# Kernel tuning notes

Hardware: AMD Instinct MI355X
Metric: run time of the kernel (lower is better)

## Reference

```python
import jax, jax.numpy as jnp
import numpy as np
import math

N = 8192
IN_FEATURES = 512
OUT_FEATURES = 64
NEG_INF = -9e15

def setup_inputs() -> dict:
    key = jax.random.key(0)
    k1, k2, k3, k4 = jax.random.split(key, 4)
    inp = jax.random.normal(k1, (N, IN_FEATURES), dtype=jnp.float32)
    adj = jax.random.randint(k2, (N, N), 0, 2, dtype=jnp.int32)
    # xavier_uniform with gain=1.414 for [in, out] weights
    limit = 1.414 * math.sqrt(6.0 / (IN_FEATURES + OUT_FEATURES))
    kW = jax.random.uniform(k3, (IN_FEATURES, OUT_FEATURES), dtype=jnp.float32, minval=-limit, maxval=limit)
    vW = jax.random.uniform(k4, (IN_FEATURES, OUT_FEATURES), dtype=jnp.float32, minval=-limit, maxval=limit)
    return {"input": inp, "adj": adj, "kW": kW, "vW": vW}

def reference(input, adj, kW, vW):
    kh = input @ kW                      # [N, d]
    vh = input @ vW                      # [N, d]
    d = kh.shape[1]
    K = (kh @ kh.T) / jnp.sqrt(jnp.asarray(d, dtype=kh.dtype))  # [N, N]
    scores = jnp.where(adj > 0, K, jnp.asarray(NEG_INF, dtype=K.dtype))
    attention = jax.nn.softmax(scores, axis=1)
    # dropout is a no-op (p=0.0 / eval mode)
    h_prime = attention @ vh             # [N, d]
    return jax.nn.elu(h_prime)           # concat=True path
```

## Files before the change

kernel.cpp:

```cpp
#include <hip/hip_runtime.h>
#include <math.h>

typedef __bf16 bf16_t;
typedef __bf16 bf16x8 __attribute__((ext_vector_type(8)));
typedef float f32x4 __attribute__((ext_vector_type(4)));

#define NN 8192
#define L2E 1.44269504088896340736f
#define SMAX 45.0f
#define KSCALE 0.35355339059327373f
#define ACCW 66

__global__ __launch_bounds__(256) void proj_kernel(
    const float* __restrict__ input,
    const float* __restrict__ kW,
    const float* __restrict__ vW,
    bf16_t* __restrict__ khs_hi,
    bf16_t* __restrict__ khs_lo,
    bf16_t* __restrict__ vhT)
{
    __shared__ __align__(16) bf16_t WkH[64][136];
    __shared__ __align__(16) bf16_t WkL[64][136];
    __shared__ __align__(16) bf16_t WvH[64][136];
    __shared__ __align__(16) bf16_t WvL[64][136];

    const int tid   = threadIdx.x;
    const int wv    = tid >> 6;
    const int lane  = tid & 63;
    const int l15   = lane & 15;
    const int quad  = lane >> 4;
    const int rbase = blockIdx.x * 64 + wv * 16;

    f32x4 kacc[4] = {};
    f32x4 vacc[4] = {};

    for (int kk = 0; kk < 4; ++kk) {
        __syncthreads();
        #pragma unroll
        for (int i = 0; i < 32; ++i) {
            int idx = tid + i * 256;
            int kl  = idx >> 6;
            int n   = idx & 63;
            float wk  = kW[(kk * 128 + kl) * 64 + n];
            float wv2 = vW[(kk * 128 + kl) * 64 + n];
            bf16_t kh = (bf16_t)wk;
            bf16_t vh = (bf16_t)wv2;
            WkH[n][kl] = kh;  WkL[n][kl] = (bf16_t)(wk - (float)kh);
            WvH[n][kl] = vh;  WvL[n][kl] = (bf16_t)(wv2 - (float)vh);
        }
        __syncthreads();

        #pragma unroll
        for (int kc = 0; kc < 4; ++kc) {
            const float* ap = &input[(size_t)(rbase + l15) * 512 + kk * 128 + kc * 32 + quad * 8];
            f32x4 a0 = *(const f32x4*)ap;
            f32x4 a1 = *(const f32x4*)(ap + 4);
            bf16x8 ah, al;
            #pragma unroll
            for (int j = 0; j < 4; ++j) {
                bf16_t h0 = (bf16_t)a0[j], h1 = (bf16_t)a1[j];
                ah[j]     = h0;  al[j]     = (bf16_t)(a0[j] - (float)h0);
                ah[4 + j] = h1;  al[4 + j] = (bf16_t)(a1[j] - (float)h1);
            }
            #pragma unroll
            for (int nb = 0; nb < 4; ++nb) {
                bf16x8 bkh = *(const bf16x8*)&WkH[nb * 16 + l15][kc * 32 + quad * 8];
                bf16x8 bkl = *(const bf16x8*)&WkL[nb * 16 + l15][kc * 32 + quad * 8];
                bf16x8 bvh = *(const bf16x8*)&WvH[nb * 16 + l15][kc * 32 + quad * 8];
                bf16x8 bvl = *(const bf16x8*)&WvL[nb * 16 + l15][kc * 32 + quad * 8];
                kacc[nb] = __builtin_amdgcn_mfma_f32_16x16x32_bf16(ah, bkh, kacc[nb], 0, 0, 0);
                kacc[nb] = __builtin_amdgcn_mfma_f32_16x16x32_bf16(al, bkh, kacc[nb], 0, 0, 0);
                kacc[nb] = __builtin_amdgcn_mfma_f32_16x16x32_bf16(ah, bkl, kacc[nb], 0, 0, 0);
                vacc[nb] = __builtin_amdgcn_mfma_f32_16x16x32_bf16(ah, bvh, vacc[nb], 0, 0, 0);
                vacc[nb] = __builtin_amdgcn_mfma_f32_16x16x32_bf16(al, bvh, vacc[nb], 0, 0, 0);
                vacc[nb] = __builtin_amdgcn_mfma_f32_16x16x32_bf16(ah, bvl, vacc[nb], 0, 0, 0);
            }
        }
    }

    #pragma unroll
    for (int nb = 0; nb < 4; ++nb) {
        const int dcol = nb * 16 + l15;
        #pragma unroll
        for (int r = 0; r < 4; ++r) {
            float v  = kacc[nb][r] * KSCALE;
            bf16_t h = (bf16_t)v;
            khs_hi[(size_t)(rbase + quad * 4 + r) * 64 + dcol] = h;
            khs_lo[(size_t)(rbase + quad * 4 + r) * 64 + dcol] = (bf16_t)(v - (float)h);
        }
        union { bf16_t b[4]; uint2 u; } pk;
        #pragma unroll
        for (int r = 0; r < 4; ++r) pk.b[r] = (bf16_t)vacc[nb][r];
        *(uint2*)&vhT[(size_t)dcol * NN + rbase + quad * 4] = pk.u;
    }
}

__global__ void zero_acc(float* __restrict__ acc) {
    int i = blockIdx.x * blockDim.x + threadIdx.x;
    if (i < NN * ACCW) acc[i] = 0.f;
}

__global__ __launch_bounds__(512, 4) void attn_kernel(
    const int* __restrict__ adj,
    const bf16_t* __restrict__ khs_hi,
    const bf16_t* __restrict__ khs_lo,
    const bf16_t* __restrict__ vhT,
    float* __restrict__ acc)
{
    __shared__ __align__(16) float PlBuf[8 * 1152];

    const int tid   = threadIdx.x;
    const int w     = tid >> 6;
    const int lane  = tid & 63;
    const int l15   = lane & 15;
    const int quad  = lane >> 4;
    const int rb    = blockIdx.x >> 1;
    const int ch    = blockIdx.x & 1;
    const int qbase = rb * 16;
    const int colstart = ch * 4096 + w * 512;

    const bf16x8 qh0 = *(const bf16x8*)&khs_hi[(size_t)(qbase + l15) * 64 + quad * 8];
    const bf16x8 qh1 = *(const bf16x8*)&khs_hi[(size_t)(qbase + l15) * 64 + 32 + quad * 8];
    const bf16x8 ql0 = *(const bf16x8*)&khs_lo[(size_t)(qbase + l15) * 64 + quad * 8];
    const bf16x8 ql1 = *(const bf16x8*)&khs_lo[(size_t)(qbase + l15) * 64 + 32 + quad * 8];

    bf16x8 ones;
    #pragma unroll
    for (int j = 0; j < 8; ++j) ones[j] = (bf16_t)1.0f;

    f32x4 o0 = {}, o1 = {}, o2 = {}, o3 = {}, o4 = {};

    const int* aptr = adj + (size_t)(qbase + quad * 4) * NN + colstart + l15;

    int acur[8], anxt[8];
    #pragma unroll
    for (int r = 0; r < 4; ++r) {
        acur[2 * r]     = aptr[(size_t)r * NN];
        acur[2 * r + 1] = aptr[(size_t)r * NN + 16];
    }

    for (int t = 0; t < 16; ++t) {
        const int colbase = colstart + t * 32;
        float* Plw = &PlBuf[w * 1152 + (t & 1) * 576];

        const bf16_t* kph = khs_hi + (size_t)(colbase + l15) * 64 + quad * 8;
        bf16x8 bh00 = *(const bf16x8*)(kph);
        bf16x8 bh01 = *(const bf16x8*)(kph + 32);
        bf16x8 bh10 = *(const bf16x8*)(kph + 16 * 64);
        bf16x8 bh11 = *(const bf16x8*)(kph + 16 * 64 + 32);
        const bf16_t* vp = vhT + (size_t)l15 * NN + colbase + quad * 8;
        bf16x8 bv0 = *(const bf16x8*)(vp);
        bf16x8 bv1 = *(const bf16x8*)(vp + (size_t)16 * NN);
        bf16x8 bv2 = *(const bf16x8*)(vp + (size_t)32 * NN);
        bf16x8 bv3 = *(const bf16x8*)(vp + (size_t)48 * NN);

        const int cnx = ((t + 1) & 15) * 32;
        #pragma unroll
        for (int r = 0; r < 4; ++r) {
            anxt[2 * r]     = aptr[(size_t)r * NN + cnx];
            anxt[2 * r + 1] = aptr[(size_t)r * NN + cnx + 16];
        }

        f32x4 zz = {};
        f32x4 s0 = __builtin_amdgcn_mfma_f32_16x16x32_bf16(qh0, bh00, zz, 0, 0, 0);
        s0 = __builtin_amdgcn_mfma_f32_16x16x32_bf16(qh1, bh01, s0, 0, 0, 0);
        s0 = __builtin_amdgcn_mfma_f32_16x16x32_bf16(ql0, bh00, s0, 0, 0, 0);
        s0 = __builtin_amdgcn_mfma_f32_16x16x32_bf16(ql1, bh01, s0, 0, 0, 0);
        f32x4 s1 = __builtin_amdgcn_mfma_f32_16x16x32_bf16(qh0, bh10, zz, 0, 0, 0);
        s1 = __builtin_amdgcn_mfma_f32_16x16x32_bf16(qh1, bh11, s1, 0, 0, 0);
        s1 = __builtin_amdgcn_mfma_f32_16x16x32_bf16(ql0, bh10, s1, 0, 0, 0);
        s1 = __builtin_amdgcn_mfma_f32_16x16x32_bf16(ql1, bh11, s1, 0, 0, 0);

        #pragma unroll
        for (int r = 0; r < 4; ++r) {
            float p0 = acur[2 * r]     > 0 ? __builtin_amdgcn_exp2f((s0[r] - SMAX) * L2E) : 0.f;
            float p1 = acur[2 * r + 1] > 0 ? __builtin_amdgcn_exp2f((s1[r] - SMAX) * L2E) : 0.f;
            Plw[(quad * 4 + r) * 36 + l15]      = p0;
            Plw[(quad * 4 + r) * 36 + 16 + l15] = p1;
        }

        __asm__ __volatile__("s_waitcnt lgkmcnt(0)" ::: "memory");

        f32x4 pfa = *(const f32x4*)&Plw[l15 * 36 + quad * 8];
        f32x4 pfb = *(const f32x4*)&Plw[l15 * 36 + quad * 8 + 4];
        bf16x8 pa;
        #pragma unroll
        for (int j = 0; j < 4; ++j) { pa[j] = (bf16_t)pfa[j]; pa[4 + j] = (bf16_t)pfb[j]; }

        o0 = __builtin_amdgcn_mfma_f32_16x16x32_bf16(pa, bv0, o0, 0, 0, 0);
        o1 = __builtin_amdgcn_mfma_f32_16x16x32_bf16(pa, bv1, o1, 0, 0, 0);
        o2 = __builtin_amdgcn_mfma_f32_16x16x32_bf16(pa, bv2, o2, 0, 0, 0);
        o3 = __builtin_amdgcn_mfma_f32_16x16x32_bf16(pa, bv3, o3, 0, 0, 0);
        o4 = __builtin_amdgcn_mfma_f32_16x16x32_bf16(pa, ones, o4, 0, 0, 0);

        #pragma unroll
        for (int i = 0; i < 8; ++i) acur[i] = anxt[i];
    }

    float* M = PlBuf;
    #pragma unroll
    for (int s = 4; s >= 1; s >>= 1) {
        __syncthreads();
        if (w >= s && w < 2 * s) {
            float* base = M + (w - s) * 16 * 68;
            #pragma unroll
            for (int r = 0; r < 4; ++r) {
                const int row = quad * 4 + r;
                base[row * 68 + l15]      = o0[r];
                base[row * 68 + 16 + l15] = o1[r];
                base[row * 68 + 32 + l15] = o2[r];
                base[row * 68 + 48 + l15] = o3[r];
                if (l15 == 0) base[row * 68 + 64] = o4[r];
            }
        }
        __syncthreads();
        if (w < s) {
            float* base = M + w * 16 * 68;
            #pragma unroll
            for (int r = 0; r < 4; ++r) {
                const int row = quad * 4 + r;
                o0[r] += base[row * 68 + l15];
                o1[r] += base[row * 68 + 16 + l15];
                o2[r] += base[row * 68 + 32 + l15];
                o3[r] += base[row * 68 + 48 + l15];
                o4[r] += base[row * 68 + 64];
            }
        }
    }

    if (w == 0) {
        #pragma unroll
        for (int r = 0; r < 4; ++r) {
            const size_t row = (size_t)qbase + quad * 4 + r;
            atomicAdd(&acc[row * ACCW + l15],      o0[r]);
            atomicAdd(&acc[row * ACCW + 16 + l15], o1[r]);
            atomicAdd(&acc[row * ACCW + 32 + l15], o2[r]);
            atomicAdd(&acc[row * ACCW + 48 + l15], o3[r]);
            if (l15 == 0) atomicAdd(&acc[row * ACCW + 64], o4[r]);
        }
    }
}

__global__ void finalize(const float* __restrict__ acc, float* __restrict__ out) {
    int i = blockIdx.x * blockDim.x + threadIdx.x;
    int row = i >> 6, d = i & 63;
    float l = acc[(size_t)row * ACCW + 64];
    float v = acc[(size_t)row * ACCW + d] / (l > 0.f ? l : 1.f);
    out[i] = v > 0.f ? v : expm1f(v);
}

extern "C" void kernel_launch(void* const* d_in, const int* in_sizes, int n_in,
                              void* d_out, int out_size, void* d_ws, size_t ws_size,
                              hipStream_t stream) {
    const float* input = nullptr;
    const int*   adj   = nullptr;
    const float* kW    = nullptr;
    const float* vW    = nullptr;
    for (int i = 0; i < n_in; ++i) {
        if (in_sizes[i] == 8192 * 512)            input = (const float*)d_in[i];
        else if (in_sizes[i] == 512 * 64) {
            if (!kW) kW = (const float*)d_in[i]; else vW = (const float*)d_in[i];
        } else                                    adj = (const int*)d_in[i];
    }
    float* out = (float*)d_out;

    bf16_t* khs_hi = (bf16_t*)d_ws;
    bf16_t* khs_lo = khs_hi + (size_t)NN * 64;
    bf16_t* vhT    = khs_lo + (size_t)NN * 64;
    float*  acc    = (float*)((char*)d_ws + 3u * 1024 * 1024);

    zero_acc<<<(NN * ACCW + 255) / 256, 256, 0, stream>>>(acc);
    proj_kernel<<<128, 256, 0, stream>>>(input, kW, vW, khs_hi, khs_lo, vhT);
    attn_kernel<<<1024, 512, 0, stream>>>(adj, khs_hi, khs_lo, vhT, acc);
    finalize<<<(NN * 64) / 512, 512, 0, stream>>>(acc, out);
}
```

Before: 517.7 us.

## Pack adjacency into bitmask, drop split-K atomics and fuse finalize into attention

Adds a pre-pass kernel that ballots the int32 adjacency matrix into a 1-bit-per-entry mask. The attention kernel then reads 32 mask bits per word instead of 32 int32 values. The attention grid no longer splits columns across two blocks: each block's 8 waves cover all 8192 columns. That removes the zero-init kernel, the global float atomics and the separate finalize kernel, and the normalization and ELU now run in the epilogue. The projection kernel moves to 128-thread blocks over 32 rows. The trade-off is an extra full pass over the adjacency matrix, plus half as many attention blocks, each with twice the serial work, which may lower occupancy.

```diff
diff --git a/kernel.cpp b/kernel.cpp
--- a/kernel.cpp
+++ b/kernel.cpp
@@ -9,9 +9,27 @@
 #define L2E 1.44269504088896340736f
 #define SMAX 45.0f
 #define KSCALE 0.35355339059327373f
-#define ACCW 66
-
-__global__ __launch_bounds__(256) void proj_kernel(
+
+__global__ __launch_bounds__(256) void pack_adj(
+    const int* __restrict__ adj, unsigned int* __restrict__ bits)
+{
+    const int lane = threadIdx.x & 63;
+    const int gw   = blockIdx.x * 4 + (threadIdx.x >> 6);
+    const int nw   = gridDim.x * 4;
+    const int nchunks = (NN / 256) * NN;
+    for (int c = gw; c < nchunks; c += nw) {
+        const int* p = adj + (size_t)c * 256;
+        unsigned int* o = bits + (size_t)c * 8;
+        #pragma unroll
+        for (int k = 0; k < 4; ++k) {
+            int v = p[k * 64 + lane];
+            unsigned long long m = __ballot(v > 0);
+            if (lane == 0) *(uint2*)(o + 2 * k) = *(uint2*)&m;
+        }
+    }
+}
+
+__global__ __launch_bounds__(128) void proj_kernel(
     const float* __restrict__ input,
     const float* __restrict__ kW,
     const float* __restrict__ vW,
@@ -29,16 +47,16 @@
     const int lane  = tid & 63;
     const int l15   = lane & 15;
     const int quad  = lane >> 4;
-    const int rbase = blockIdx.x * 64 + wv * 16;
+    const int rbase = blockIdx.x * 32 + wv * 16;
 
     f32x4 kacc[4] = {};
     f32x4 vacc[4] = {};
 
     for (int kk = 0; kk < 4; ++kk) {
         __syncthreads();
-        #pragma unroll
-        for (int i = 0; i < 32; ++i) {
-            int idx = tid + i * 256;
+        #pragma unroll 16
+        for (int i = 0; i < 64; ++i) {
+            int idx = tid + i * 128;
             int kl  = idx >> 6;
             int n   = idx & 63;
             float wk  = kW[(kk * 128 + kl) * 64 + n];
@@ -95,17 +113,12 @@
     }
 }
 
-__global__ void zero_acc(float* __restrict__ acc) {
-    int i = blockIdx.x * blockDim.x + threadIdx.x;
-    if (i < NN * ACCW) acc[i] = 0.f;
-}
-
 __global__ __launch_bounds__(512, 4) void attn_kernel(
-    const int* __restrict__ adj,
+    const unsigned int* __restrict__ bits,
     const bf16_t* __restrict__ khs_hi,
     const bf16_t* __restrict__ khs_lo,
     const bf16_t* __restrict__ vhT,
-    float* __restrict__ acc)
+    float* __restrict__ out)
 {
     __shared__ __align__(16) float PlBuf[8 * 1152];
 
@@ -114,10 +127,8 @@
     const int lane  = tid & 63;
     const int l15   = lane & 15;
     const int quad  = lane >> 4;
-    const int rb    = blockIdx.x >> 1;
-    const int ch    = blockIdx.x & 1;
-    const int qbase = rb * 16;
-    const int colstart = ch * 4096 + w * 512;
+    const int qbase = blockIdx.x * 16;
+    const int colstart = w * 1024;
 
     const bf16x8 qh0 = *(const bf16x8*)&khs_hi[(size_t)(qbase + l15) * 64 + quad * 8];
     const bf16x8 qh1 = *(const bf16x8*)&khs_hi[(size_t)(qbase + l15) * 64 + 32 + quad * 8];
@@ -130,16 +141,13 @@
 
     f32x4 o0 = {}, o1 = {}, o2 = {}, o3 = {}, o4 = {};
 
-    const int* aptr = adj + (size_t)(qbase + quad * 4) * NN + colstart + l15;
-
-    int acur[8], anxt[8];
-    #pragma unroll
-    for (int r = 0; r < 4; ++r) {
-        acur[2 * r]     = aptr[(size_t)r * NN];
-        acur[2 * r + 1] = aptr[(size_t)r * NN + 16];
-    }
-
-    for (int t = 0; t < 16; ++t) {
+    const unsigned int* bp = bits + (size_t)(qbase + quad * 4) * 256 + (colstart >> 5);
+
+    unsigned int wcur[4], wnxt[4];
+    #pragma unroll
+    for (int r = 0; r < 4; ++r) wcur[r] = bp[r * 256];
+
+    for (int t = 0; t < 32; ++t) {
         const int colbase = colstart + t * 32;
         float* Plw = &PlBuf[w * 1152 + (t & 1) * 576];
 
@@ -154,12 +162,9 @@
         bf16x8 bv2 = *(const bf16x8*)(vp + (size_t)32 * NN);
         bf16x8 bv3 = *(const bf16x8*)(vp + (size_t)48 * NN);
 
-        const int cnx = ((t + 1) & 15) * 32;
-        #pragma unroll
-        for (int r = 0; r < 4; ++r) {
-            anxt[2 * r]     = aptr[(size_t)r * NN + cnx];
-            anxt[2 * r + 1] = aptr[(size_t)r * NN + cnx + 16];
-        }
+        const int tn = (t + 1) & 31;
+        #pragma unroll
+        for (int r = 0; r < 4; ++r) wnxt[r] = bp[r * 256 + tn];
 
         f32x4 zz = {};
         f32x4 s0 = __builtin_amdgcn_mfma_f32_16x16x32_bf16(qh0, bh00, zz, 0, 0, 0);
@@ -173,8 +178,8 @@
 
         #pragma unroll
         for (int r = 0; r < 4; ++r) {
-            float p0 = acur[2 * r]     > 0 ? __builtin_amdgcn_exp2f((s0[r] - SMAX) * L2E) : 0.f;
-            float p1 = acur[2 * r + 1] > 0 ? __builtin_amdgcn_exp2f((s1[r] - SMAX) * L2E) : 0.f;
+            float p0 = ((wcur[r] >> l15) & 1u)        ? __builtin_amdgcn_exp2f((s0[r] - SMAX) * L2E) : 0.f;
+            float p1 = ((wcur[r] >> (16 + l15)) & 1u) ? __builtin_amdgcn_exp2f((s1[r] - SMAX) * L2E) : 0.f;
             Plw[(quad * 4 + r) * 36 + l15]      = p0;
             Plw[(quad * 4 + r) * 36 + 16 + l15] = p1;
         }
@@ -194,7 +199,7 @@
         o4 = __builtin_amdgcn_mfma_f32_16x16x32_bf16(pa, ones, o4, 0, 0, 0);
 
         #pragma unroll
-        for (int i = 0; i < 8; ++i) acur[i] = anxt[i];
+        for (int r = 0; r < 4; ++r) wcur[r] = wnxt[r];
     }
 
     float* M = PlBuf;
@@ -232,21 +237,15 @@
         #pragma unroll
         for (int r = 0; r < 4; ++r) {
             const size_t row = (size_t)qbase + quad * 4 + r;
-            atomicAdd(&acc[row * ACCW + l15],      o0[r]);
-            atomicAdd(&acc[row * ACCW + 16 + l15], o1[r]);
-            atomicAdd(&acc[row * ACCW + 32 + l15], o2[r]);
-            atomicAdd(&acc[row * ACCW + 48 + l15], o3[r]);
-            if (l15 == 0) atomicAdd(&acc[row * ACCW + 64], o4[r]);
-        }
-    }
-}
-
-__global__ void finalize(const float* __restrict__ acc, float* __restrict__ out) {
-    int i = blockIdx.x * blockDim.x + threadIdx.x;
-    int row = i >> 6, d = i & 63;
-    float l = acc[(size_t)row * ACCW + 64];
-    float v = acc[(size_t)row * ACCW + d] / (l > 0.f ? l : 1.f);
-    out[i] = v > 0.f ? v : expm1f(v);
+            float l   = o4[r];
+            float inv = 1.0f / (l > 0.f ? l : 1.0f);
+            float v0 = o0[r] * inv, v1 = o1[r] * inv, v2 = o2[r] * inv, v3 = o3[r] * inv;
+            out[row * 64 + l15]      = v0 > 0.f ? v0 : expm1f(v0);
+            out[row * 64 + 16 + l15] = v1 > 0.f ? v1 : expm1f(v1);
+            out[row * 64 + 32 + l15] = v2 > 0.f ? v2 : expm1f(v2);
+            out[row * 64 + 48 + l15] = v3 > 0.f ? v3 : expm1f(v3);
+        }
+    }
 }
 
 extern "C" void kernel_launch(void* const* d_in, const int* in_sizes, int n_in,
@@ -267,10 +266,9 @@
     bf16_t* khs_hi = (bf16_t*)d_ws;
     bf16_t* khs_lo = khs_hi + (size_t)NN * 64;
     bf16_t* vhT    = khs_lo + (size_t)NN * 64;
-    float*  acc    = (float*)((char*)d_ws + 3u * 1024 * 1024);
-
-    zero_acc<<<(NN * ACCW + 255) / 256, 256, 0, stream>>>(acc);
-    proj_kernel<<<128, 256, 0, stream>>>(input, kW, vW, khs_hi, khs_lo, vhT);
-    attn_kernel<<<1024, 512, 0, stream>>>(adj, khs_hi, khs_lo, vhT, acc);
-    finalize<<<(NN * 64) / 512, 512, 0, stream>>>(acc, out);
-}
+    unsigned int* bits = (unsigned int*)((char*)d_ws + 3u * 1024 * 1024);
+
+    pack_adj<<<2048, 256, 0, stream>>>(adj, bits);
+    proj_kernel<<<256, 128, 0, stream>>>(input, kW, vW, khs_hi, khs_lo, vhT);
+    attn_kernel<<<512, 512, 0, stream>>>(bits, khs_hi, khs_lo, vhT, out);
+}
```

After: 531.5 us. +2.7%, slower.
